# Performance work log

Hardware: AMD Instinct MI355X
Metric: run time of the kernel (lower is better)

## Reference

```python
import jax, jax.numpy as jnp
import numpy as np

EPS = 1e-6
BETA = 0.25
COMMIT_W = 1.0


def setup_inputs() -> dict:
    key = jax.random.key(0)
    k1, k2, k3 = jax.random.split(key, 3)
    b, c, h, w = 8, 256, 32, 32
    n_e, e_dim = 16384, 256
    z = jax.random.normal(k1, (b, c, h, w), jnp.float32)
    # frozen_codebook = randn(n_e, e_dim) * e_dim**-0.5
    codebook = jax.random.normal(k2, (n_e, e_dim), jnp.float32) * (e_dim ** -0.5)
    # nn.Linear(e_dim, in_channels, bias=False) weight: (in_channels, e_dim)
    W = jax.random.normal(k3, (c, e_dim), jnp.float32) * (e_dim ** -0.5)
    return {"z": z, "codebook": codebook, "W": W}


def _rotate_to(src, tgt):
    # Rotation trick (Fifty et al.): rotate src onto tgt direction with a
    # detached Householder-style transform; gradient flows through src only.
    # src, tgt: (n, d)
    norm_src = jnp.linalg.norm(src, axis=-1, keepdims=True)
    norm_tgt = jnp.linalg.norm(tgt, axis=-1, keepdims=True)
    u = src / (norm_src + EPS)
    q = tgt / (norm_tgt + EPS)
    uq = u + q
    w_ = jax.lax.stop_gradient(uq / (jnp.linalg.norm(uq, axis=-1, keepdims=True) + EPS))
    u_d = jax.lax.stop_gradient(u)
    q_d = jax.lax.stop_gradient(q)
    rot = (src
           - 2.0 * jnp.sum(src * w_, axis=-1, keepdims=True) * w_
           + 2.0 * jnp.sum(src * u_d, axis=-1, keepdims=True) * q_d)
    return rot * jax.lax.stop_gradient(norm_tgt / (norm_src + EPS))


def reference(z, codebook, W):
    b, c, h, w = z.shape
    # b c h w -> (b*h*w, c)
    z_flat = jnp.transpose(z, (0, 2, 3, 1)).reshape(-1, c)
    # implicit codebook: frozen codes through linear projection
    emb = codebook @ W.T  # (n_e, c)
    # squared L2 distances (no grad needed for argmin)
    d = (jnp.sum(z_flat ** 2, axis=1, keepdims=True)
         + jnp.sum(emb ** 2, axis=1)
         - 2.0 * (z_flat @ emb.T))  # (n_tok, n_e)
    indices = jnp.argmin(d, axis=1)  # (n_tok,)
    z_q_flat = emb[indices]  # gather quantized vectors
    loss = COMMIT_W * (jnp.mean((jax.lax.stop_gradient(z_flat) - z_q_flat) ** 2)
                       + BETA * jnp.mean((z_flat - jax.lax.stop_gradient(z_q_flat)) ** 2))
    z_q_flat = _rotate_to(z_flat, z_q_flat)
    z_q = jnp.transpose(z_q_flat.reshape(b, h, w, c), (0, 3, 1, 2))
    return z_q, loss, indices
```

## Files before the change

kernel.cpp:

```cpp
#include <hip/hip_runtime.h>
#include <math.h>

#define EPSV 1e-6f
#define NTOK 8192
#define NE   16384
#define DIM  256

using short8 = __attribute__((ext_vector_type(8))) short;
using f32x4v = __attribute__((ext_vector_type(4))) float;

__device__ __forceinline__ unsigned short f2bf(float v) {
    unsigned int u = __float_as_uint(v);
    u += 0x7fffu + ((u >> 16) & 1u);
    return (unsigned short)(u >> 16);
}
__device__ __forceinline__ float bf2f(unsigned short h) {
    return __uint_as_float(((unsigned int)h) << 16);
}

__device__ __forceinline__ void gload_lds16(const void* g, void* s) {
    __builtin_amdgcn_global_load_lds(
        (const __attribute__((address_space(1))) void*)g,
        (__attribute__((address_space(3))) void*)s, 16, 0, 0);
}

__device__ __forceinline__ void split8(const float4 a, const float4 b,
                                       short8& h, short8& l) {
    float f[8] = {a.x, a.y, a.z, a.w, b.x, b.y, b.z, b.w};
#pragma unroll
    for (int j = 0; j < 8; ++j) {
        unsigned short hh = f2bf(f[j]);
        h[j] = (short)hh;
        l[j] = (short)f2bf(f[j] - bf2f(hh));
    }
}

__global__ __launch_bounds__(256) void f1_pre(
    const float* __restrict__ zin, float* __restrict__ z_flat,
    unsigned short* __restrict__ zh, unsigned short* __restrict__ zl,
    float* __restrict__ sz, const float* __restrict__ Wm,
    unsigned short* __restrict__ wh, unsigned short* __restrict__ wl) {
    const int bid = blockIdx.x;
    const int tid = threadIdx.x;
    if (bid >= 128) {
        const int i = ((bid - 128) * 256 + tid) * 4;
        const float4 v = *(const float4*)(Wm + i);
        float f[4] = {v.x, v.y, v.z, v.w};
#pragma unroll
        for (int j = 0; j < 4; ++j) {
            unsigned short h = f2bf(f[j]);
            wh[i + j] = h;
            wl[i + j] = f2bf(f[j] - bf2f(h));
        }
        return;
    }
    __shared__ float tile[64][65];
    const int yx0 = (bid & 15) * 64, b = bid >> 4;
    const int sub = tid >> 6, ln = tid & 63;
    double dacc[16];
#pragma unroll
    for (int j = 0; j < 16; ++j) dacc[j] = 0.0;

    for (int cc = 0; cc < 4; ++cc) {
        const int c0 = cc * 64;
        __syncthreads();
#pragma unroll
        for (int j = 0; j < 16; ++j) {
            int cl = j * 4 + sub;
            tile[cl][ln] = zin[((size_t)(b * 256 + c0 + cl) << 10) + yx0 + ln];
        }
        __syncthreads();
#pragma unroll
        for (int j = 0; j < 16; ++j) {
            int tl = j * 4 + sub;
            float v = tile[ln][tl];
            size_t o = (size_t)(b * 1024 + yx0 + tl) * 256 + c0 + ln;
            z_flat[o] = v;
            unsigned short h = f2bf(v);
            zh[o] = h;
            zl[o] = f2bf(v - bf2f(h));
            dacc[j] += (double)v * v;
        }
    }
#pragma unroll
    for (int j = 0; j < 16; ++j) {
        double s = dacc[j];
#pragma unroll
        for (int m = 1; m < 64; m <<= 1) s += __shfl_xor(s, m);
        if (ln == 0) sz[b * 1024 + yx0 + j * 4 + sub] = (float)s;
    }
}

__global__ __launch_bounds__(256, 2) void k0c_emb(
    const float* __restrict__ cb, const unsigned short* __restrict__ wh,
    const unsigned short* __restrict__ wl, float* __restrict__ emb,
    unsigned short* __restrict__ eh, unsigned short* __restrict__ el,
    float* __restrict__ se0, float* __restrict__ se1) {
    __shared__ char smemC[65536];
    const int tid = threadIdx.x;
    const int w = tid >> 6, lane = tid & 63;
    const int quad = lane >> 4, lr = lane & 15;
    const int wr = w & 1, wc = w >> 1;
    const int n0 = blockIdx.x * 128, c0 = blockIdx.y * 128;

    f32x4v acc[4][4];
#pragma unroll
    for (int mt = 0; mt < 4; ++mt)
#pragma unroll
        for (int nt = 0; nt < 4; ++nt)
            acc[mt][nt] = (f32x4v){0.f, 0.f, 0.f, 0.f};

    for (int kc = 0; kc < 4; ++kc) {
        __syncthreads();
#pragma unroll
        for (int i = 0; i < 16; ++i) {
            int s = i * 4 + w;
            int u = s * 64 + lane;
            const void* g;
            if (s < 32) {
                int kg = u >> 7, row = u & 127;
                g = cb + (size_t)(n0 + row) * 256 + kc * 64 + kg * 4;
            } else if (s < 48) {
                int u1 = u - 2048;
                int kg = u1 >> 7, row = u1 & 127;
                g = wh + (size_t)(c0 + row) * 256 + kc * 64 + kg * 8;
            } else {
                int u2 = u - 3072;
                int kg = u2 >> 7, row = u2 & 127;
                g = wl + (size_t)(c0 + row) * 256 + kc * 64 + kg * 8;
            }
            gload_lds16(g, smemC + ((size_t)u << 4));
        }
        __syncthreads();
#pragma unroll
        for (int ks = 0; ks < 2; ++ks) {
            short8 Ah[4], Al[4], Bh[4], Bl[4];
#pragma unroll
            for (int mt = 0; mt < 4; ++mt) {
                int m = wr * 64 + mt * 16 + lr;
                int kg2 = ks * 8 + quad * 2;
                float4 f0 = *(const float4*)(smemC + (((size_t)kg2 * 128 + m) << 4));
                float4 f1 = *(const float4*)(smemC + ((((size_t)kg2 + 1) * 128 + m) << 4));
                split8(f0, f1, Ah[mt], Al[mt]);
            }
#pragma unroll
            for (int nt = 0; nt < 4; ++nt) {
                int n = wc * 64 + nt * 16 + lr;
                int ku = (ks * 4 + quad) * 128 + n;
                Bh[nt] = *(const short8*)(smemC + (((size_t)2048 + ku) << 4));
                Bl[nt] = *(const short8*)(smemC + (((size_t)3072 + ku) << 4));
            }
#pragma unroll
            for (int mt = 0; mt < 4; ++mt)
#pragma unroll
                for (int nt = 0; nt < 4; ++nt) {
                    f32x4v a = acc[mt][nt];
                    a = __builtin_amdgcn_mfma_f32_16x16x32_bf16(Ah[mt], Bh[nt], a, 0, 0, 0);
                    a = __builtin_amdgcn_mfma_f32_16x16x32_bf16(Ah[mt], Bl[nt], a, 0, 0, 0);
                    a = __builtin_amdgcn_mfma_f32_16x16x32_bf16(Al[mt], Bh[nt], a, 0, 0, 0);
                    a = __builtin_amdgcn_mfma_f32_16x16x32_bf16(Al[mt], Bl[nt], a, 0, 0, 0);
                    acc[mt][nt] = a;
                }
        }
    }
#pragma unroll
    for (int mt = 0; mt < 4; ++mt)
#pragma unroll
        for (int rr = 0; rr < 4; ++rr) {
            int row = n0 + wr * 64 + mt * 16 + quad * 4 + rr;
#pragma unroll
            for (int nt = 0; nt < 4; ++nt) {
                int col = c0 + wc * 64 + nt * 16 + lr;
                size_t o = (size_t)row * 256 + col;
                float v = acc[mt][nt][rr];
                emb[o] = v;
                unsigned short h = f2bf(v);
                eh[o] = h;
                el[o] = f2bf(v - bf2f(h));
            }
        }
    __syncthreads();
    float* sblk = (float*)smemC;
#pragma unroll
    for (int mt = 0; mt < 4; ++mt)
#pragma unroll
        for (int rr = 0; rr < 4; ++rr) {
            float s = 0.f;
#pragma unroll
            for (int nt = 0; nt < 4; ++nt) {
                float v = acc[mt][nt][rr];
                s = fmaf(v, v, s);
            }
#pragma unroll
            for (int st = 1; st < 16; st <<= 1) s += __shfl_xor(s, st);
            if (lr == 0)
                sblk[wc * 128 + wr * 64 + mt * 16 + quad * 4 + rr] = s;
        }
    __syncthreads();
    if (tid < 128) {
        float* sep = (blockIdx.y == 0) ? se0 : se1;
        sep[n0 + tid] = sblk[tid] + sblk[128 + tid];
    }
}

__global__ __launch_bounds__(512, 4) void k1_dist_argmin(
    const unsigned short* __restrict__ zh, const unsigned short* __restrict__ zl,
    const unsigned short* __restrict__ eh, const unsigned short* __restrict__ el,
    const float* __restrict__ sz, const float* __restrict__ se0,
    const float* __restrict__ se1, float* __restrict__ pval,
    int* __restrict__ pidx) {
    __shared__ short8 smem[2][2048];
    __shared__ float seS[2048];
    const int tid = threadIdx.x;
    const int w = tid >> 6, lane = tid & 63;
    const int quad = lane >> 4, lr = lane & 15;
    const int bid = blockIdx.x;
    const int slab = bid & 7;
    const int rowBase = (bid >> 3) * 128 + w * 16;
    const int slabBase = slab * 2048;

    for (int j = tid; j < 2048; j += 512)
        seS[j] = __fadd_rn(se0[slabBase + j], se1[slabBase + j]);

    short8 Ah[8], Al[8];
#pragma unroll
    for (int ks = 0; ks < 8; ++ks) {
        size_t o = (size_t)(rowBase + lr) * 256 + ks * 32 + quad * 8;
        Ah[ks] = *(const short8*)(zh + o);
        Al[ks] = *(const short8*)(zl + o);
    }

    float szr[4];
#pragma unroll
    for (int rr = 0; rr < 4; ++rr)
        szr[rr] = sz[rowBase + quad * 4 + rr];

    float minv[4];
    int mini[4];
#pragma unroll
    for (int rr = 0; rr < 4; ++rr) {
        minv[rr] = INFINITY;
        mini[rr] = 0;
    }

    const unsigned short* gp[4];
#pragma unroll
    for (int i = 0; i < 4; ++i) {
        int u = i * 512 + tid;
        int fmt = u >> 10;
        int u1 = u & 1023;
        int col = u1 >> 5, kgs = u1 & 31;
        int kg = kgs ^ col;
        gp[i] = (fmt ? el : eh) + (size_t)(slabBase + col) * 256 + kg * 8;
    }

    auto stage = [&](int buf, int ch) {
        const int off = ch << 13;
#pragma unroll
        for (int i = 0; i < 4; ++i) {
            gload_lds16(gp[i] + off, (char*)&smem[0][0] + buf * 32768 +
                                         (((size_t)i * 512 + w * 64) << 4));
        }
    };

    auto compute_ep = [&](int cur, int ch) {
        f32x4v acc0 = (f32x4v){0.f, 0.f, 0.f, 0.f};
        f32x4v acc1 = (f32x4v){0.f, 0.f, 0.f, 0.f};
        const int col0 = lr, col1 = 16 + lr;
#pragma unroll
        for (int ks = 0; ks < 8; ++ks) {
            const int kq = ks * 4 + quad;
            const int k0 = kq ^ col0, k1i = kq ^ col1;
            short8 Bh0 = smem[cur][col0 * 32 + k0];
            short8 Bl0 = smem[cur][1024 + col0 * 32 + k0];
            short8 Bh1 = smem[cur][col1 * 32 + k1i];
            short8 Bl1 = smem[cur][1024 + col1 * 32 + k1i];
            acc0 = __builtin_amdgcn_mfma_f32_16x16x32_bf16(Ah[ks], Bh0, acc0, 0, 0, 0);
            acc1 = __builtin_amdgcn_mfma_f32_16x16x32_bf16(Ah[ks], Bh1, acc1, 0, 0, 0);
            acc0 = __builtin_amdgcn_mfma_f32_16x16x32_bf16(Ah[ks], Bl0, acc0, 0, 0, 0);
            acc1 = __builtin_amdgcn_mfma_f32_16x16x32_bf16(Ah[ks], Bl1, acc1, 0, 0, 0);
            acc0 = __builtin_amdgcn_mfma_f32_16x16x32_bf16(Al[ks], Bh0, acc0, 0, 0, 0);
            acc1 = __builtin_amdgcn_mfma_f32_16x16x32_bf16(Al[ks], Bh1, acc1, 0, 0, 0);
        }
        const int base = ch * 32;
        {
            const int colg = slabBase + base + lr;
            const float sec = seS[base + lr];
#pragma unroll
            for (int rr = 0; rr < 4; ++rr) {
                float szse = __fadd_rn(szr[rr], sec);
                float d = fmaf(-2.0f, acc0[rr], szse);
                if (d < minv[rr]) { minv[rr] = d; mini[rr] = colg; }
            }
        }
        {
            const int colg = slabBase + base + 16 + lr;
            const float sec = seS[base + 16 + lr];
#pragma unroll
            for (int rr = 0; rr < 4; ++rr) {
                float szse = __fadd_rn(szr[rr], sec);
                float d = fmaf(-2.0f, acc1[rr], szse);
                if (d < minv[rr]) { minv[rr] = d; mini[rr] = colg; }
            }
        }
    };

    stage(0, 0);
    __syncthreads();

#pragma unroll 1
    for (int ch = 0; ch < 64; ch += 2) {
        stage(1, ch + 1);
        compute_ep(0, ch);
        __syncthreads();
        if (ch + 2 < 64) stage(0, ch + 2);
        compute_ep(1, ch + 1);
        __syncthreads();
    }

#pragma unroll
    for (int st = 1; st < 16; st <<= 1) {
#pragma unroll
        for (int rr = 0; rr < 4; ++rr) {
            float ov = __shfl_xor(minv[rr], st);
            int oi = __shfl_xor(mini[rr], st);
            if (ov < minv[rr] ||
                (ov == minv[rr] && oi < mini[rr])) {
                minv[rr] = ov;
                mini[rr] = oi;
            }
        }
    }
    if (lr == 0) {
#pragma unroll
        for (int rr = 0; rr < 4; ++rr) {
            int row = rowBase + quad * 4 + rr;
            pval[(size_t)row * 8 + slab] = minv[rr];
            pidx[(size_t)row * 8 + slab] = mini[rr];
        }
    }
}

__global__ __launch_bounds__(256) void k3a_token(
    const float* __restrict__ z_flat, const float* __restrict__ emb,
    const float* __restrict__ pval, const int* __restrict__ pidx,
    float* __restrict__ alpha, float* __restrict__ beta,
    int* __restrict__ idxf, float* __restrict__ out,
    float* __restrict__ lpart) {
    __shared__ float red[4];
    const int w = threadIdx.x >> 6, lane = threadIdx.x & 63;
    const int t = blockIdx.x * 4 + w;

    float bv = INFINITY;
    int bi = 0x7fffffff;
    if (lane < 8) {
        bv = pval[(size_t)t * 8 + lane];
        bi = pidx[(size_t)t * 8 + lane];
    }
#pragma unroll
    for (int st = 1; st < 8; st <<= 1) {
        float ov = __shfl_xor(bv, st);
        int oi = __shfl_xor(bi, st);
        if (ov < bv || (ov == bv && oi < bi)) { bv = ov; bi = oi; }
    }
    const int best = __shfl(bi, 0);

    const float4 zv = *(const float4*)(z_flat + (size_t)t * 256 + lane * 4);
    const float4 ev = *(const float4*)(emb + (size_t)best * 256 + lane * 4);
    float szs = zv.x * zv.x + zv.y * zv.y + zv.z * zv.z + zv.w * zv.w;
    float ses = ev.x * ev.x + ev.y * ev.y + ev.z * ev.z + ev.w * ev.w;
    float zes = zv.x * ev.x + zv.y * ev.y + zv.z * ev.z + zv.w * ev.w;
    float dx = zv.x - ev.x, dy = zv.y - ev.y, dz = zv.z - ev.z, dw = zv.w - ev.w;
    float sqs = dx * dx + dy * dy + dz * dz + dw * dw;
#pragma unroll
    for (int m = 1; m < 64; m <<= 1) {
        szs += __shfl_xor(szs, m);
        ses += __shfl_xor(ses, m);
        zes += __shfl_xor(zes, m);
        sqs += __shfl_xor(sqs, m);
    }
    if (lane == 0) {
        float ns = sqrtf(szs), nt = sqrtf(ses);
        float inv_s = 1.0f / (ns + EPSV);
        float inv_t = 1.0f / (nt + EPSV);
        float s2 = szs * inv_s;
        float su = szs * inv_s * inv_s;
        float sq = ses * inv_t * inv_t;
        float uq = zes * inv_s * inv_t;
        float nw = sqrtf(su + sq + 2.0f * uq);
        float inv_w = 1.0f / (nw + EPSV);
        float s1 = (s2 + zes * inv_t) * inv_w;
        float scale = nt * inv_s;
        float a = scale * (1.0f - 2.0f * s1 * inv_w * inv_s);
        float bb = scale * inv_t * 2.0f * (s2 - s1 * inv_w);
        alpha[t] = a;
        beta[t] = bb;
        idxf[t] = best;
        out[2097153 + t] = (float)best;
        red[w] = sqs;
    }
    __syncthreads();
    if (threadIdx.x == 0)
        lpart[blockIdx.x] = red[0] + red[1] + red[2] + red[3];
}

__global__ __launch_bounds__(256) void k3b_zq(
    const float* __restrict__ zin, const float* __restrict__ emb,
    const float* __restrict__ alpha, const float* __restrict__ beta,
    const int* __restrict__ idxf, const float* __restrict__ lpart,
    float* __restrict__ out) {
    if (blockIdx.x == 0) {
        __shared__ float red[4];
        const int tid = threadIdx.x;
        float s = 0.0f;
        for (int i = tid; i < 2048; i += 256) s += lpart[i];
#pragma unroll
        for (int m = 1; m < 64; m <<= 1) s += __shfl_xor(s, m);
        if ((tid & 63) == 0) red[tid >> 6] = s;
        __syncthreads();
        if (tid == 0)
            out[2097152] = 1.25f * (red[0] + red[1] + red[2] + red[3]) *
                           (1.0f / 2097152.0f);
    }
    const int i = blockIdx.x * 256 + threadIdx.x;
    const int c = (i >> 10) & 255;
    const int t = ((i >> 18) << 10) | (i & 1023);
    out[i] = alpha[t] * zin[i] + beta[t] * emb[(size_t)idxf[t] * 256 + c];
}

extern "C" void kernel_launch(void* const* d_in, const int* in_sizes, int n_in,
                              void* d_out, int out_size, void* d_ws,
                              size_t ws_size, hipStream_t stream) {
    (void)in_sizes; (void)n_in; (void)out_size; (void)ws_size;
    const float* zin = (const float*)d_in[0];
    const float* cb  = (const float*)d_in[1];
    const float* Wm  = (const float*)d_in[2];
    float* out = (float*)d_out;
    char* ws = (char*)d_ws;

    float*          z_flat = (float*)(ws + 0);
    unsigned short* zh     = (unsigned short*)(ws + 8388608);
    unsigned short* zl     = (unsigned short*)(ws + 12582912);
    float*          emb    = (float*)(ws + 16777216);
    unsigned short* eh     = (unsigned short*)(ws + 33554432);
    unsigned short* el     = (unsigned short*)(ws + 41943040);
    float*          sz     = (float*)(ws + 50331648);
    float*          se0    = (float*)(ws + 50364416);
    float*          se1    = (float*)(ws + 50429952);
    float*          pval   = (float*)(ws + 50495488);
    int*            pidx   = (int*)(ws + 50757632);
    float*          alpha  = (float*)(ws + 51019776);
    float*          beta   = (float*)(ws + 51052544);
    int*            idxf   = (int*)(ws + 51085312);
    float*          lpart  = (float*)(ws + 51118080);
    unsigned short* wh     = (unsigned short*)(ws + 51126272);
    unsigned short* wl     = (unsigned short*)(ws + 51257344);

    f1_pre<<<192, 256, 0, stream>>>(zin, z_flat, zh, zl, sz, Wm, wh, wl);
    k0c_emb<<<dim3(128, 2), 256, 0, stream>>>(cb, wh, wl, emb, eh, el,
                                              se0, se1);
    k1_dist_argmin<<<512, 512, 0, stream>>>(zh, zl, eh, el, sz,
                                            se0, se1, pval, pidx);
    k3a_token<<<2048, 256, 0, stream>>>(z_flat, emb, pval, pidx, alpha, beta,
                                        idxf, out, lpart);
    k3b_zq<<<8192, 256, 0, stream>>>(zin, emb, alpha, beta, idxf, lpart, out);
}
```

Baseline: 304.4 us.

## Switch distance GEMM to 32x32x16 MFMA with 32 rows per wave

The distance/argmin kernel now uses 32x32x16 bf16 MFMAs, so each wave covers 32 token rows against 32 codebook columns instead of 16 rows. This halves the number of blocks and roughly halves the LDS traffic for codebook tiles per token row. Two accumulators split the K dimension and are summed before the argmin epilogue. In exchange, register use goes up (more A fragments and 16-element accumulators), occupancy drops to 2 blocks per CU, and the grid shrinks to 256 blocks, which may underfill the GPU's CUs.

```diff
diff --git a/kernel.cpp b/kernel.cpp
--- a/kernel.cpp
+++ b/kernel.cpp
@@ -8,6 +8,7 @@
 
 using short8 = __attribute__((ext_vector_type(8))) short;
 using f32x4v = __attribute__((ext_vector_type(4))) float;
+using f32x16 = __attribute__((ext_vector_type(16))) float;
 
 __device__ __forceinline__ unsigned short f2bf(float v) {
     unsigned int u = __float_as_uint(v);
@@ -203,7 +204,7 @@
     }
 }
 
-__global__ __launch_bounds__(512, 4) void k1_dist_argmin(
+__global__ __launch_bounds__(512, 2) void k1_dist_argmin(
     const unsigned short* __restrict__ zh, const unsigned short* __restrict__ zl,
     const unsigned short* __restrict__ eh, const unsigned short* __restrict__ el,
     const float* __restrict__ sz, const float* __restrict__ se0,
@@ -213,34 +214,34 @@
     __shared__ float seS[2048];
     const int tid = threadIdx.x;
     const int w = tid >> 6, lane = tid & 63;
-    const int quad = lane >> 4, lr = lane & 15;
+    const int cl = lane & 31, hi = lane >> 5;
     const int bid = blockIdx.x;
     const int slab = bid & 7;
-    const int rowBase = (bid >> 3) * 128 + w * 16;
+    const int rowBase = (bid >> 3) * 256 + w * 32;
     const int slabBase = slab * 2048;
 
     for (int j = tid; j < 2048; j += 512)
         seS[j] = __fadd_rn(se0[slabBase + j], se1[slabBase + j]);
 
-    short8 Ah[8], Al[8];
-#pragma unroll
-    for (int ks = 0; ks < 8; ++ks) {
-        size_t o = (size_t)(rowBase + lr) * 256 + ks * 32 + quad * 8;
+    short8 Ah[16], Al[16];
+#pragma unroll
+    for (int ks = 0; ks < 16; ++ks) {
+        size_t o = (size_t)(rowBase + cl) * 256 + ks * 16 + hi * 8;
         Ah[ks] = *(const short8*)(zh + o);
         Al[ks] = *(const short8*)(zl + o);
     }
 
-    float szr[4];
-#pragma unroll
-    for (int rr = 0; rr < 4; ++rr)
-        szr[rr] = sz[rowBase + quad * 4 + rr];
-
-    float minv[4];
-    int mini[4];
-#pragma unroll
-    for (int rr = 0; rr < 4; ++rr) {
-        minv[rr] = INFINITY;
-        mini[rr] = 0;
+    float szr[16];
+#pragma unroll
+    for (int r = 0; r < 16; ++r)
+        szr[r] = sz[rowBase + (r & 3) + 8 * (r >> 2) + 4 * hi];
+
+    float minv[16];
+    int mini[16];
+#pragma unroll
+    for (int r = 0; r < 16; ++r) {
+        minv[r] = INFINITY;
+        mini[r] = 0;
     }
 
     const unsigned short* gp[4];
@@ -264,43 +265,39 @@
     };
 
     auto compute_ep = [&](int cur, int ch) {
-        f32x4v acc0 = (f32x4v){0.f, 0.f, 0.f, 0.f};
-        f32x4v acc1 = (f32x4v){0.f, 0.f, 0.f, 0.f};
-        const int col0 = lr, col1 = 16 + lr;
-#pragma unroll
-        for (int ks = 0; ks < 8; ++ks) {
-            const int kq = ks * 4 + quad;
-            const int k0 = kq ^ col0, k1i = kq ^ col1;
-            short8 Bh0 = smem[cur][col0 * 32 + k0];
-            short8 Bl0 = smem[cur][1024 + col0 * 32 + k0];
-            short8 Bh1 = smem[cur][col1 * 32 + k1i];
-            short8 Bl1 = smem[cur][1024 + col1 * 32 + k1i];
-            acc0 = __builtin_amdgcn_mfma_f32_16x16x32_bf16(Ah[ks], Bh0, acc0, 0, 0, 0);
-            acc1 = __builtin_amdgcn_mfma_f32_16x16x32_bf16(Ah[ks], Bh1, acc1, 0, 0, 0);
-            acc0 = __builtin_amdgcn_mfma_f32_16x16x32_bf16(Ah[ks], Bl0, acc0, 0, 0, 0);
-            acc1 = __builtin_amdgcn_mfma_f32_16x16x32_bf16(Ah[ks], Bl1, acc1, 0, 0, 0);
-            acc0 = __builtin_amdgcn_mfma_f32_16x16x32_bf16(Al[ks], Bh0, acc0, 0, 0, 0);
-            acc1 = __builtin_amdgcn_mfma_f32_16x16x32_bf16(Al[ks], Bh1, acc1, 0, 0, 0);
-        }
-        const int base = ch * 32;
-        {
-            const int colg = slabBase + base + lr;
-            const float sec = seS[base + lr];
-#pragma unroll
-            for (int rr = 0; rr < 4; ++rr) {
-                float szse = __fadd_rn(szr[rr], sec);
-                float d = fmaf(-2.0f, acc0[rr], szse);
-                if (d < minv[rr]) { minv[rr] = d; mini[rr] = colg; }
-            }
-        }
-        {
-            const int colg = slabBase + base + 16 + lr;
-            const float sec = seS[base + 16 + lr];
-#pragma unroll
-            for (int rr = 0; rr < 4; ++rr) {
-                float szse = __fadd_rn(szr[rr], sec);
-                float d = fmaf(-2.0f, acc1[rr], szse);
-                if (d < minv[rr]) { minv[rr] = d; mini[rr] = colg; }
+        f32x16 accE = {0.f, 0.f, 0.f, 0.f, 0.f, 0.f, 0.f, 0.f,
+                       0.f, 0.f, 0.f, 0.f, 0.f, 0.f, 0.f, 0.f};
+        f32x16 accO = {0.f, 0.f, 0.f, 0.f, 0.f, 0.f, 0.f, 0.f,
+                       0.f, 0.f, 0.f, 0.f, 0.f, 0.f, 0.f, 0.f};
+#pragma unroll
+        for (int kp = 0; kp < 8; ++kp) {
+            {
+                const int kg = (4 * kp + hi) ^ cl;
+                short8 Bh = smem[cur][cl * 32 + kg];
+                short8 Bl = smem[cur][1024 + cl * 32 + kg];
+                accE = __builtin_amdgcn_mfma_f32_32x32x16_bf16(Ah[2 * kp], Bh, accE, 0, 0, 0);
+                accE = __builtin_amdgcn_mfma_f32_32x32x16_bf16(Ah[2 * kp], Bl, accE, 0, 0, 0);
+                accE = __builtin_amdgcn_mfma_f32_32x32x16_bf16(Al[2 * kp], Bh, accE, 0, 0, 0);
+            }
+            {
+                const int kg = (4 * kp + 2 + hi) ^ cl;
+                short8 Bh = smem[cur][cl * 32 + kg];
+                short8 Bl = smem[cur][1024 + cl * 32 + kg];
+                accO = __builtin_amdgcn_mfma_f32_32x32x16_bf16(Ah[2 * kp + 1], Bh, accO, 0, 0, 0);
+                accO = __builtin_amdgcn_mfma_f32_32x32x16_bf16(Ah[2 * kp + 1], Bl, accO, 0, 0, 0);
+                accO = __builtin_amdgcn_mfma_f32_32x32x16_bf16(Al[2 * kp + 1], Bh, accO, 0, 0, 0);
+            }
+        }
+        const int colg = slabBase + ch * 32 + cl;
+        const float sec = seS[ch * 32 + cl];
+#pragma unroll
+        for (int r = 0; r < 16; ++r) {
+            float dot = __fadd_rn(accE[r], accO[r]);
+            float szse = __fadd_rn(szr[r], sec);
+            float d = fmaf(-2.0f, dot, szse);
+            if (d < minv[r]) {
+                minv[r] = d;
+                mini[r] = colg;
             }
         }
     };
@@ -319,24 +316,24 @@
     }
 
 #pragma unroll
-    for (int st = 1; st < 16; st <<= 1) {
-#pragma unroll
-        for (int rr = 0; rr < 4; ++rr) {
-            float ov = __shfl_xor(minv[rr], st);
-            int oi = __shfl_xor(mini[rr], st);
-            if (ov < minv[rr] ||
-                (ov == minv[rr] && oi < mini[rr])) {
-                minv[rr] = ov;
-                mini[rr] = oi;
-            }
-        }
-    }
-    if (lr == 0) {
-#pragma unroll
-        for (int rr = 0; rr < 4; ++rr) {
-            int row = rowBase + quad * 4 + rr;
-            pval[(size_t)row * 8 + slab] = minv[rr];
-            pidx[(size_t)row * 8 + slab] = mini[rr];
+    for (int st = 1; st < 32; st <<= 1) {
+#pragma unroll
+        for (int r = 0; r < 16; ++r) {
+            float ov = __shfl_xor(minv[r], st);
+            int oi = __shfl_xor(mini[r], st);
+            if (ov < minv[r] ||
+                (ov == minv[r] && oi < mini[r])) {
+                minv[r] = ov;
+                mini[r] = oi;
+            }
+        }
+    }
+    if (cl == 0) {
+#pragma unroll
+        for (int r = 0; r < 16; ++r) {
+            int row = rowBase + (r & 3) + 8 * (r >> 2) + 4 * hi;
+            pval[(size_t)row * 8 + slab] = minv[r];
+            pidx[(size_t)row * 8 + slab] = mini[r];
         }
     }
 }
@@ -459,7 +456,7 @@
     f1_pre<<<192, 256, 0, stream>>>(zin, z_flat, zh, zl, sz, Wm, wh, wl);
     k0c_emb<<<dim3(128, 2), 256, 0, stream>>>(cb, wh, wl, emb, eh, el,
                                               se0, se1);
-    k1_dist_argmin<<<512, 512, 0, stream>>>(zh, zl, eh, el, sz,
+    k1_dist_argmin<<<256, 512, 0, stream>>>(zh, zl, eh, el, sz,
                                             se0, se1, pval, pidx);
     k3a_token<<<2048, 256, 0, stream>>>(z_flat, emb, pval, pidx, alpha, beta,
                                         idxf, out, lpart);
```

New measurement: 291.5 us. 4.2% less time.
